# Performance work log

Hardware: AMD Instinct MI355X
Metric: run time of the kernel (lower is better)

Reference implementation:

```python
import jax, jax.numpy as jnp
import numpy as np

EPS = 1e-12  # torch F.normalize default eps


def conv1x1(x, w, b):
    # x: [N,C,H,W], w: [K,C], b: [K]
    return jnp.einsum('nchw,kc->nkhw', x, w) + b[None, :, None, None]


def forward_sa(f1, f2, cw1, cb1, cw2, cb2):
    n, _, h, w = f1.shape
    c1 = conv1x1(f1, cw1, cb1)  # [N,1,H,W]
    c2 = conv1x1(f2, cw2, cb2)
    c1 = jax.nn.softmax(c1.reshape(n, h * w), axis=1).reshape(n, 1, h, w)
    c2 = jax.nn.softmax(c2.reshape(n, h * w), axis=1).reshape(n, 1, h, w)
    return c1 * f1, c2 * f2


def l2norm_ch(x):
    # torch F.normalize(x) -> p=2 over dim=1 with eps clamp
    n = jnp.sqrt(jnp.sum(x * x, axis=1, keepdims=True))
    return x / jnp.maximum(n, EPS)


def forward_ca(f1, f2, pw1, pb1, pw2, pb2):
    N, C, H, W = f1.shape
    f1_cl = conv1x1(f1, pw1, pb1).reshape(N, -1, H * W)  # [N,Cl,HW]
    f2_cl = conv1x1(f2, pw2, pb2).reshape(N, -1, H * W)
    # A[n,p,q] = sum_c f2_cl[n,c,p] * f1_cl[n,c,q]  -> [N,HW,HW]
    A_c = jnp.tanh(jnp.einsum('ncp,ncq->npq', f2_cl, f1_cl))
    f1_v = f1.reshape(N, C, H * W)
    f2_v = f2.reshape(N, C, H * W)
    # f1_hat = f1_v @ A_c^T ; f2_hat = f2_v @ A_c
    f1_hat = jnp.einsum('ncp,nqp->ncq', f1_v, A_c).reshape(N, C, H, W)
    f2_hat = jnp.einsum('ncp,npq->ncq', f2_v, A_c).reshape(N, C, H, W)
    return l2norm_ch(f1_hat), l2norm_ch(f2_hat)


def setup_inputs() -> dict:
    key = jax.random.key(0)
    ks = jax.random.split(key, 10)
    N, C, H, W = 2, 256, 64, 64
    Cl = C // 16
    sc = 1.0 / np.sqrt(C)
    return {
        'f1': jax.random.normal(ks[0], (N, C, H, W), jnp.float32),
        'f2': jax.random.normal(ks[1], (N, C, H, W), jnp.float32),
        'pw1': jax.random.normal(ks[2], (Cl, C), jnp.float32) * sc,
        'pb1': jax.random.normal(ks[3], (Cl,), jnp.float32) * sc,
        'pw2': jax.random.normal(ks[4], (Cl, C), jnp.float32) * sc,
        'pb2': jax.random.normal(ks[5], (Cl,), jnp.float32) * sc,
        'cw1': jax.random.normal(ks[6], (1, C), jnp.float32) * sc,
        'cb1': jax.random.normal(ks[7], (1,), jnp.float32) * sc,
        'cw2': jax.random.normal(ks[8], (1, C), jnp.float32) * sc,
        'cb2': jax.random.normal(ks[9], (1,), jnp.float32) * sc,
    }


def reference(f1, f2, pw1, pb1, pw2, pb2, cw1, cb1, cw2, cb2):
    f1_1, f2_1 = forward_sa(f1, f2, cw1, cb1, cw2, cb2)
    f1_hat, f2_hat = forward_ca(f1_1, f2_1, pw1, pb1, pw2, pb2)
    fp1_hat = jax.nn.relu(f1_hat + f1)
    fp2_hat = jax.nn.relu(f2_hat + f2)
    f1_2, f2_2 = forward_sa(fp1_hat, fp2_hat, cw1, cb1, cw2, cb2)
    # Original calls forward_ca(f1_2, f2_2) again but discards the result
    # and returns (f1_2, f2_2); the dead call is omitted (identical output).
    return (f1_2, f2_2)
```

## Files before the change

### kernel.cpp

```cpp
#include <hip/hip_runtime.h>
#include <hip/hip_bf16.h>
#include <math.h>

#define N_B 2
#define C_CH 256
#define HW_SZ 4096
#define CL_CH 16

typedef __bf16 bf16x8 __attribute__((ext_vector_type(8)));
typedef float f32x4 __attribute__((ext_vector_type(4)));
typedef float f32x16 __attribute__((ext_vector_type(16)));

__device__ __forceinline__ unsigned short f2bf(float x){
  __hip_bfloat16 b = __float2bfloat16(x);
  return *reinterpret_cast<unsigned short*>(&b);
}
__device__ __forceinline__ float bf2f(unsigned short u){
  unsigned int w = ((unsigned int)u) << 16;
  return *reinterpret_cast<float*>(&w);
}
__device__ __forceinline__ unsigned int cvtpk(float a, float b){
  unsigned int r;
  asm("v_cvt_pk_bf16_f32 %0, %1, %2" : "=v"(r) : "v"(a), "v"(b));
  return r;
}
__device__ __forceinline__ float tanh_fast(float x){
  float e = __expf(2.0f * x);
  return fmaf(-2.0f, __builtin_amdgcn_rcpf(1.0f + e), 1.0f);
}
__device__ __forceinline__ void gload16(const void* gsrc, void* lds_dst){
  __builtin_amdgcn_global_load_lds(
      (const __attribute__((address_space(1))) unsigned int*)gsrc,
      (__attribute__((address_space(3))) unsigned int*)lds_dst, 16, 0, 0);
}

__global__ void k_conv1(const float* __restrict__ f1, const float* __restrict__ f2,
                        const float* __restrict__ w1, const float* __restrict__ w2,
                        const float* __restrict__ b1, const float* __restrict__ b2,
                        float* __restrict__ cv){
  const int i = blockIdx.z, n = blockIdx.y, t = threadIdx.x;
  const int ql = t & 63, cg = t >> 6;
  const int q = blockIdx.x * 64 + ql;
  const float* f = (i ? f2 : f1) + n * C_CH * HW_SZ;
  const float* w = i ? w2 : w1;
  __shared__ float ws[C_CH];
  __shared__ float red[4][72];
  ws[t] = w[t];
  __syncthreads();
  float acc = 0.f;
  #pragma unroll 8
  for (int c = cg * 64; c < cg * 64 + 64; ++c)
    acc += f[c * HW_SZ + q] * ws[c];
  red[cg][ql] = acc;
  __syncthreads();
  if (t < 64){
    float s = red[0][t] + red[1][t] + red[2][t] + red[3][t] + (i ? b2[0] : b1[0]);
    cv[(i * 2 + n) * HW_SZ + blockIdx.x * 64 + t] = s;
  }
}

__global__ void k_scale_cl(const float* __restrict__ f1, const float* __restrict__ f2,
                           const float* __restrict__ cv,
                           const float* __restrict__ pw1, const float* __restrict__ pw2,
                           const float* __restrict__ pb1, const float* __restrict__ pb2,
                           unsigned short* __restrict__ fs1, unsigned short* __restrict__ fs2,
                           unsigned short* __restrict__ clT1, unsigned short* __restrict__ clT2){
  const int i = blockIdx.z, n = blockIdx.y, t = threadIdx.x;
  const int ql = t & 63, cg = t >> 6;
  const int q = blockIdx.x * 64 + ql;
  const float* f = (i ? f2 : f1) + n * C_CH * HW_SZ;
  unsigned short* fs = (i ? fs2 : fs1) + n * C_CH * HW_SZ;
  unsigned short* clT = (i ? clT2 : clT1) + n * 32 * HW_SZ;
  const float* pw = i ? pw2 : pw1;
  const float* pb = i ? pb2 : pb1;
  const float* cvrow = cv + (i * 2 + n) * HW_SZ;
  __shared__ float wls[CL_CH * C_CH];
  __shared__ float red[4][CL_CH][66];
  __shared__ float smr[256];
  #pragma unroll
  for (int j = 0; j < 16; j++) wls[j * 256 + t] = pw[j * 256 + t];
  float sv[16];
  float m = -1e30f;
  #pragma unroll
  for (int j = 0; j < 16; j++){ sv[j] = cvrow[j * 256 + t]; m = fmaxf(m, sv[j]); }
  smr[t] = m; __syncthreads();
  for (int s = 128; s > 0; s >>= 1){ if (t < s) smr[t] = fmaxf(smr[t], smr[t + s]); __syncthreads(); }
  m = smr[0]; __syncthreads();
  float sum = 0.f;
  #pragma unroll
  for (int j = 0; j < 16; j++) sum += __expf(sv[j] - m);
  smr[t] = sum; __syncthreads();
  for (int s = 128; s > 0; s >>= 1){ if (t < s) smr[t] += smr[t + s]; __syncthreads(); }
  const float p = __expf(cvrow[q] - m) * (1.0f / smr[0]);

  float acc[16];
  #pragma unroll
  for (int k = 0; k < 16; k++) acc[k] = 0.f;
  for (int c = cg * 64; c < cg * 64 + 64; ++c){
    float vv = f[c * HW_SZ + q] * p;
    fs[c * HW_SZ + q] = f2bf(vv);
    #pragma unroll
    for (int k = 0; k < 16; k++) acc[k] += wls[k * 256 + c] * vv;
  }
  #pragma unroll
  for (int k = 0; k < 16; k++) red[cg][k][ql] = acc[k];
  __syncthreads();
  #pragma unroll
  for (int j = 0; j < 4; j++){
    int e = j * 256 + t; int k = e >> 6, qq = e & 63;
    float s = red[0][k][qq] + red[1][k][qq] + red[2][k][qq] + red[3][k][qq] + pb[k];
    clT[(blockIdx.x * 64 + qq) * 32 + k] = f2bf(s);
  }
  if (t < 128){
    uint4 zv = {0u, 0u, 0u, 0u};
    int qq = t >> 1, half = t & 1;
    *reinterpret_cast<uint4*>(&clT[(blockIdx.x * 64 + qq) * 32 + 16 + half * 8]) = zv;
  }
}

__global__ __launch_bounds__(512, 2) void k_hat(
    const unsigned short* __restrict__ fs1, const unsigned short* __restrict__ fs2,
    const unsigned short* __restrict__ clT1, const unsigned short* __restrict__ clT2,
    float* __restrict__ hat1, float* __restrict__ hat2,
    float* __restrict__ pt1, float* __restrict__ pt2){
  const int t = threadIdx.x;
  const int bid = blockIdx.x;
  const int xcd = bid & 7, slot = bid >> 3;
  const int z = xcd >> 1;
  const int n = z & 1, i = z >> 1;
  const int x = slot * 2 + (xcd & 1);
  const int qt = x >> 1, ph = x & 1;
  const int q0 = qt * 128;
  const int pbase = ph * 2048;

  const unsigned short* fs = (i ? fs2 : fs1) + n * C_CH * HW_SZ;
  const unsigned short* uT = (i ? clT1 : clT2) + n * 32 * HW_SZ;
  const unsigned short* vT = (i ? clT2 : clT1) + n * 32 * HW_SZ;
  float* out = (ph ? (i ? pt2 : pt1) : (i ? hat2 : hat1)) + n * C_CH * HW_SZ;

  __shared__ __align__(16) unsigned short fsA[3][C_CH * 64];
  __shared__ __align__(16) unsigned short aT[3][128 * 64];

  const int wv = t >> 6, l = t & 63;
  const int g4 = l >> 4, lr16 = l & 15;
  const int g2 = l >> 5, lr32 = l & 31;

  const int pfw = wv & 3;
  const int qh  = wv >> 2;
  const int cblk = wv & 3, qblk = wv >> 2;

  bf16x8 ub[4];
  #pragma unroll
  for (int j = 0; j < 4; ++j)
    ub[j] = *reinterpret_cast<const bf16x8*>(&uT[(q0 + qh * 64 + j * 16 + lr16) * 32 + g4 * 8]);

  f32x16 acc00, acc01, acc10, acc11;
  #pragma unroll
  for (int r = 0; r < 16; ++r){ acc00[r] = 0.f; acc01[r] = 0.f; acc10[r] = 0.f; acc11[r] = 0.f; }
  const f32x4 zz = {0.f, 0.f, 0.f, 0.f};

  int fs_src[4];
  #pragma unroll
  for (int it = 0; it < 4; ++it){
    int d = it * 512 + t; int c = d >> 3, sl = d & 7;
    int u = sl ^ (c & 7) ^ (((c >> 3) & 1) << 2) ^ (((c >> 4) & 1) << 1);
    fs_src[it] = c * (HW_SZ * 2) + u * 16;
  }
  const int vgo = (pfw * 16 + lr16) * 64 + g4 * 16;
  unsigned atw0;
  {
    int qd = qh * 64 + lr16;
    int sw = (pfw * 2 + (g4 >> 1)) ^ (qd & 7) ^ (((qd >> 3) & 1) << 2);
    atw0 = qd * 128 + sw * 16 + (g4 & 1) * 8;
  }
  unsigned afo[2], bqo[2];
  #pragma unroll
  for (int cf = 0; cf < 2; ++cf){
    int crow = cblk * 64 + cf * 32 + lr32;
    afo[cf] = crow * 128 +
      ((g2 ^ (crow & 7) ^ (((crow >> 3) & 1) << 2) ^ (((crow >> 4) & 1) << 1)) << 4);
  }
  #pragma unroll
  for (int qf = 0; qf < 2; ++qf){
    int qrow = qblk * 64 + qf * 32 + lr32;
    bqo[qf] = qrow * 128 +
      ((g2 ^ (qrow & 7) ^ (((qrow >> 3) & 1) << 2) ^ (((qrow >> 4) & 1) << 1)) << 4);
  }

  auto stage_fs = [&](char* dstbase, const char* src){
    #pragma unroll
    for (int it = 0; it < 4; ++it)
      gload16(src + fs_src[it], dstbase + (it * 512 + wv * 64) * 16);
  };
  auto dgen = [&](uint4 vr, char* atB){
    bf16x8 av = *reinterpret_cast<bf16x8*>(&vr);
    #pragma unroll
    for (int j = 0; j < 4; ++j){
      f32x4 d = __builtin_amdgcn_mfma_f32_16x16x32_bf16(av, ub[j], zz, 0, 0, 0);
      uint2 pk;
      pk.x = cvtpk(tanh_fast(d[0]), tanh_fast(d[1]));
      pk.y = cvtpk(tanh_fast(d[2]), tanh_fast(d[3]));
      unsigned off = (atw0 + (unsigned)(j * 2048)) ^ ((unsigned)(j & 1) << 5);
      *reinterpret_cast<uint2*>(atB + off) = pk;
    }
  };
  auto mmain = [&](const char* faB, const char* atB){
    __builtin_amdgcn_s_setprio(1);
    #pragma unroll
    for (int ks = 0; ks < 4; ++ks){
      unsigned kx = (unsigned)(ks << 5);
      bf16x8 a0 = *reinterpret_cast<const bf16x8*>(faB + (afo[0] ^ kx));
      bf16x8 a1 = *reinterpret_cast<const bf16x8*>(faB + (afo[1] ^ kx));
      bf16x8 b0 = *reinterpret_cast<const bf16x8*>(atB + (bqo[0] ^ kx));
      bf16x8 b1 = *reinterpret_cast<const bf16x8*>(atB + (bqo[1] ^ kx));
      acc00 = __builtin_amdgcn_mfma_f32_32x32x16_bf16(a0, b0, acc00, 0, 0, 0);
      acc01 = __builtin_amdgcn_mfma_f32_32x32x16_bf16(a0, b1, acc01, 0, 0, 0);
      acc10 = __builtin_amdgcn_mfma_f32_32x32x16_bf16(a1, b0, acc10, 0, 0, 0);
      acc11 = __builtin_amdgcn_mfma_f32_32x32x16_bf16(a1, b1, acc11, 0, 0, 0);
    }
    __builtin_amdgcn_s_setprio(0);
  };

  const char* fpp = (const char*)fs + pbase * 2;
  const char* vp  = (const char*)vT + pbase * 64 + vgo;

  char *fRd = (char*)&fsA[0][0], *fWr = (char*)&fsA[1][0], *fSp = (char*)&fsA[2][0];
  char *aRd = (char*)&aT[0][0],  *aWr = (char*)&aT[1][0],  *aSp = (char*)&aT[2][0];

  stage_fs(fRd, fpp); fpp += 128;
  uint4 vb;
  {
    uint4 va = *reinterpret_cast<const uint4*>(vp);
    vb = *reinterpret_cast<const uint4*>(vp + 4096);
    vp += 8192;
    dgen(va, aRd);
  }

  #pragma unroll 1
  for (int k = 0; k < 32; ++k){
    stage_fs(fWr, fpp); fpp += 128;
    uint4 vnew = *reinterpret_cast<const uint4*>(vp); vp += 4096;
    dgen(vb, aWr);
    vb = vnew;
    asm volatile("s_waitcnt lgkmcnt(0)" ::: "memory");
    __builtin_amdgcn_sched_barrier(0);
    __builtin_amdgcn_s_barrier();
    __builtin_amdgcn_sched_barrier(0);
    mmain(fRd, aRd);
    char* tf = fRd; fRd = fWr; fWr = fSp; fSp = tf;
    char* ta = aRd; aRd = aWr; aWr = aSp; aSp = ta;
  }

  const int qcol = q0 + qblk * 64 + lr32;
  #pragma unroll
  for (int r = 0; r < 16; ++r){
    int cr = (r & 3) + 8 * (r >> 2) + 4 * g2;
    out[(cblk * 64 + cr) * HW_SZ + qcol] = acc00[r];
    out[(cblk * 64 + cr) * HW_SZ + qcol + 32] = acc01[r];
    out[(cblk * 64 + 32 + cr) * HW_SZ + qcol] = acc10[r];
    out[(cblk * 64 + 32 + cr) * HW_SZ + qcol + 32] = acc11[r];
  }
}

__global__ void k_norm(const float* __restrict__ hat1, const float* __restrict__ hat2,
                       const float* __restrict__ pt1, const float* __restrict__ pt2,
                       const float* __restrict__ f1, const float* __restrict__ f2,
                       const float* __restrict__ cw1, const float* __restrict__ cw2,
                       const float* __restrict__ cb1, const float* __restrict__ cb2,
                       unsigned short* __restrict__ fpb1, unsigned short* __restrict__ fpb2,
                       float* __restrict__ cv2){
  const int i = blockIdx.z, n = blockIdx.y, t = threadIdx.x;
  const int ql = t & 63, cg = t >> 6;
  const int q = blockIdx.x * 64 + ql;
  const float* hat = (i ? hat2 : hat1) + n * C_CH * HW_SZ;
  const float* pt = (i ? pt2 : pt1) + n * C_CH * HW_SZ;
  const float* f = (i ? f2 : f1) + n * C_CH * HW_SZ;
  unsigned short* fpb = (i ? fpb2 : fpb1) + n * C_CH * HW_SZ;
  __shared__ float ws[C_CH];
  __shared__ float red[4][72];
  __shared__ float invs[64];
  __shared__ unsigned short hLs[C_CH][66];
  ws[t] = (i ? cw2 : cw1)[t];
  __syncthreads();
  float s = 0.f;
  #pragma unroll 8
  for (int c = cg * 64; c < cg * 64 + 64; ++c){
    float h = hat[c * HW_SZ + q] + pt[c * HW_SZ + q];
    hLs[c][ql] = f2bf(h);
    s += h * h;
  }
  red[cg][ql] = s; __syncthreads();
  if (t < 64){
    float ss = red[0][t] + red[1][t] + red[2][t] + red[3][t];
    invs[t] = 1.0f / fmaxf(sqrtf(ss), 1e-12f);
  }
  __syncthreads();
  const float inv = invs[ql];
  float ca = 0.f;
  #pragma unroll 8
  for (int c = cg * 64; c < cg * 64 + 64; ++c){
    float vv = fmaxf(bf2f(hLs[c][ql]) * inv + f[c * HW_SZ + q], 0.0f);
    fpb[c * HW_SZ + q] = f2bf(vv);
    ca += ws[c] * vv;
  }
  red[cg][ql] = ca; __syncthreads();
  if (t < 64){
    float ss = red[0][t] + red[1][t] + red[2][t] + red[3][t] + (i ? cb2[0] : cb1[0]);
    cv2[(i * 2 + n) * HW_SZ + blockIdx.x * 64 + t] = ss;
  }
}

__global__ void k_final(const unsigned short* __restrict__ fp1,
                        const unsigned short* __restrict__ fp2,
                        const float* __restrict__ cv2, float* __restrict__ outp){
  const int i = blockIdx.z, t = threadIdx.x;
  const int idx4 = (blockIdx.x * 256 + t) * 4;
  const int n = idx4 >> 20;
  const int q = idx4 & (HW_SZ - 1);
  const float* cvrow = cv2 + (i * 2 + n) * HW_SZ;
  __shared__ float red[256];
  float sv[16];
  float m = -1e30f;
  #pragma unroll
  for (int j = 0; j < 16; j++){ sv[j] = cvrow[j * 256 + t]; m = fmaxf(m, sv[j]); }
  red[t] = m; __syncthreads();
  for (int s = 128; s > 0; s >>= 1){ if (t < s) red[t] = fmaxf(red[t], red[t + s]); __syncthreads(); }
  m = red[0]; __syncthreads();
  float sum = 0.f;
  #pragma unroll
  for (int j = 0; j < 16; j++) sum += __expf(sv[j] - m);
  red[t] = sum; __syncthreads();
  for (int s = 128; s > 0; s >>= 1){ if (t < s) red[t] += red[t + s]; __syncthreads(); }
  const float invS = 1.0f / red[0];

  const unsigned short* fp = i ? fp2 : fp1;
  ushort4 vv = *reinterpret_cast<const ushort4*>(&fp[idx4]);
  float4 o;
  o.x = bf2f(vv.x) * (__expf(cvrow[q + 0] - m) * invS);
  o.y = bf2f(vv.y) * (__expf(cvrow[q + 1] - m) * invS);
  o.z = bf2f(vv.z) * (__expf(cvrow[q + 2] - m) * invS);
  o.w = bf2f(vv.w) * (__expf(cvrow[q + 3] - m) * invS);
  *reinterpret_cast<float4*>(&outp[i * (C_CH * HW_SZ * N_B) + idx4]) = o;
}

extern "C" void kernel_launch(void* const* d_in, const int* in_sizes, int n_in,
                              void* d_out, int out_size, void* d_ws, size_t ws_size,
                              hipStream_t stream){
  const float* f1  = (const float*)d_in[0];
  const float* f2  = (const float*)d_in[1];
  const float* pw1 = (const float*)d_in[2];
  const float* pb1 = (const float*)d_in[3];
  const float* pw2 = (const float*)d_in[4];
  const float* pb2 = (const float*)d_in[5];
  const float* cw1 = (const float*)d_in[6];
  const float* cb1 = (const float*)d_in[7];
  const float* cw2 = (const float*)d_in[8];
  const float* cb2 = (const float*)d_in[9];
  float* ws = (float*)d_ws;
  float* HAT1 = ws;
  float* HAT2 = ws + 2097152;
  float* PT1  = ws + 4194304;
  float* PT2  = ws + 6291456;
  unsigned short* FS1 = (unsigned short*)(ws + 8388608);
  unsigned short* FS2 = (unsigned short*)(ws + 9437184);
  unsigned short* CLT1 = (unsigned short*)(ws + 10485760);
  unsigned short* CLT2 = (unsigned short*)(ws + 10616832);
  float* CV1  = ws + 10747904;
  float* CV2  = ws + 10764288;
  float* outp = (float*)d_out;
  unsigned short* FPB1 = FS1;
  unsigned short* FPB2 = FS2;

  k_conv1   <<<dim3(64, 2, 2), 256, 0, stream>>>(f1, f2, cw1, cw2, cb1, cb2, CV1);
  k_scale_cl<<<dim3(64, 2, 2), 256, 0, stream>>>(f1, f2, CV1, pw1, pw2, pb1, pb2,
                                                 FS1, FS2, CLT1, CLT2);
  k_hat     <<<256, 512, 0, stream>>>(FS1, FS2, CLT1, CLT2, HAT1, HAT2, PT1, PT2);
  k_norm    <<<dim3(64, 2, 2), 256, 0, stream>>>(HAT1, HAT2, PT1, PT2, f1, f2,
                                                 cw1, cw2, cb1, cb2, FPB1, FPB2, CV2);
  k_final   <<<dim3(2048, 1, 2), 256, 0, stream>>>(FPB1, FPB2, CV2, outp);
}
```

Measured before the change: 96.72 us.

## Store hat partials as bf16 and reorder MFMA before dgen in k_hat loop

The k_hat partial outputs (hat and pt) are now written and read as bf16 instead of fp32, which halves the intermediate HBM traffic between k_hat and k_norm. The main loop is reordered so that mmain on the current buffers runs before generating the next attention tile, with an extra barrier before the loop. The s_setprio hints are removed. Storing partials in bf16 adds rounding error before they are summed, and the reordering changes how MFMA work overlaps with tanh and LDS writes.

```diff
diff --git a/kernel.cpp b/kernel.cpp
--- a/kernel.cpp
+++ b/kernel.cpp
@@ -121,8 +121,8 @@
 __global__ __launch_bounds__(512, 2) void k_hat(
     const unsigned short* __restrict__ fs1, const unsigned short* __restrict__ fs2,
     const unsigned short* __restrict__ clT1, const unsigned short* __restrict__ clT2,
-    float* __restrict__ hat1, float* __restrict__ hat2,
-    float* __restrict__ pt1, float* __restrict__ pt2){
+    unsigned short* __restrict__ hat1, unsigned short* __restrict__ hat2,
+    unsigned short* __restrict__ pt1, unsigned short* __restrict__ pt2){
   const int t = threadIdx.x;
   const int bid = blockIdx.x;
   const int xcd = bid & 7, slot = bid >> 3;
@@ -136,7 +136,7 @@
   const unsigned short* fs = (i ? fs2 : fs1) + n * C_CH * HW_SZ;
   const unsigned short* uT = (i ? clT1 : clT2) + n * 32 * HW_SZ;
   const unsigned short* vT = (i ? clT2 : clT1) + n * 32 * HW_SZ;
-  float* out = (ph ? (i ? pt2 : pt1) : (i ? hat2 : hat1)) + n * C_CH * HW_SZ;
+  unsigned short* out = (ph ? (i ? pt2 : pt1) : (i ? hat2 : hat1)) + n * C_CH * HW_SZ;
 
   __shared__ __align__(16) unsigned short fsA[3][C_CH * 64];
   __shared__ __align__(16) unsigned short aT[3][128 * 64];
@@ -205,7 +205,6 @@
     }
   };
   auto mmain = [&](const char* faB, const char* atB){
-    __builtin_amdgcn_s_setprio(1);
     #pragma unroll
     for (int ks = 0; ks < 4; ++ks){
       unsigned kx = (unsigned)(ks << 5);
@@ -218,7 +217,6 @@
       acc10 = __builtin_amdgcn_mfma_f32_32x32x16_bf16(a1, b0, acc10, 0, 0, 0);
       acc11 = __builtin_amdgcn_mfma_f32_32x32x16_bf16(a1, b1, acc11, 0, 0, 0);
     }
-    __builtin_amdgcn_s_setprio(0);
   };
 
   const char* fpp = (const char*)fs + pbase * 2;
@@ -235,18 +233,22 @@
     vp += 8192;
     dgen(va, aRd);
   }
+  asm volatile("s_waitcnt lgkmcnt(0)" ::: "memory");
+  __builtin_amdgcn_sched_barrier(0);
+  __builtin_amdgcn_s_barrier();
+  __builtin_amdgcn_sched_barrier(0);
 
   #pragma unroll 1
   for (int k = 0; k < 32; ++k){
     stage_fs(fWr, fpp); fpp += 128;
     uint4 vnew = *reinterpret_cast<const uint4*>(vp); vp += 4096;
+    mmain(fRd, aRd);
     dgen(vb, aWr);
     vb = vnew;
     asm volatile("s_waitcnt lgkmcnt(0)" ::: "memory");
     __builtin_amdgcn_sched_barrier(0);
     __builtin_amdgcn_s_barrier();
     __builtin_amdgcn_sched_barrier(0);
-    mmain(fRd, aRd);
     char* tf = fRd; fRd = fWr; fWr = fSp; fSp = tf;
     char* ta = aRd; aRd = aWr; aWr = aSp; aSp = ta;
   }
@@ -255,15 +257,17 @@
   #pragma unroll
   for (int r = 0; r < 16; ++r){
     int cr = (r & 3) + 8 * (r >> 2) + 4 * g2;
-    out[(cblk * 64 + cr) * HW_SZ + qcol] = acc00[r];
-    out[(cblk * 64 + cr) * HW_SZ + qcol + 32] = acc01[r];
-    out[(cblk * 64 + 32 + cr) * HW_SZ + qcol] = acc10[r];
-    out[(cblk * 64 + 32 + cr) * HW_SZ + qcol + 32] = acc11[r];
-  }
-}
-
-__global__ void k_norm(const float* __restrict__ hat1, const float* __restrict__ hat2,
-                       const float* __restrict__ pt1, const float* __restrict__ pt2,
+    out[(cblk * 64 + cr) * HW_SZ + qcol] = f2bf(acc00[r]);
+    out[(cblk * 64 + cr) * HW_SZ + qcol + 32] = f2bf(acc01[r]);
+    out[(cblk * 64 + 32 + cr) * HW_SZ + qcol] = f2bf(acc10[r]);
+    out[(cblk * 64 + 32 + cr) * HW_SZ + qcol + 32] = f2bf(acc11[r]);
+  }
+}
+
+__global__ void k_norm(const unsigned short* __restrict__ hat1,
+                       const unsigned short* __restrict__ hat2,
+                       const unsigned short* __restrict__ pt1,
+                       const unsigned short* __restrict__ pt2,
                        const float* __restrict__ f1, const float* __restrict__ f2,
                        const float* __restrict__ cw1, const float* __restrict__ cw2,
                        const float* __restrict__ cb1, const float* __restrict__ cb2,
@@ -272,8 +276,8 @@
   const int i = blockIdx.z, n = blockIdx.y, t = threadIdx.x;
   const int ql = t & 63, cg = t >> 6;
   const int q = blockIdx.x * 64 + ql;
-  const float* hat = (i ? hat2 : hat1) + n * C_CH * HW_SZ;
-  const float* pt = (i ? pt2 : pt1) + n * C_CH * HW_SZ;
+  const unsigned short* hat = (i ? hat2 : hat1) + n * C_CH * HW_SZ;
+  const unsigned short* pt = (i ? pt2 : pt1) + n * C_CH * HW_SZ;
   const float* f = (i ? f2 : f1) + n * C_CH * HW_SZ;
   unsigned short* fpb = (i ? fpb2 : fpb1) + n * C_CH * HW_SZ;
   __shared__ float ws[C_CH];
@@ -285,7 +289,7 @@
   float s = 0.f;
   #pragma unroll 8
   for (int c = cg * 64; c < cg * 64 + 64; ++c){
-    float h = hat[c * HW_SZ + q] + pt[c * HW_SZ + q];
+    float h = bf2f(hat[c * HW_SZ + q]) + bf2f(pt[c * HW_SZ + q]);
     hLs[c][ql] = f2bf(h);
     s += h * h;
   }
@@ -357,16 +361,16 @@
   const float* cw2 = (const float*)d_in[8];
   const float* cb2 = (const float*)d_in[9];
   float* ws = (float*)d_ws;
-  float* HAT1 = ws;
-  float* HAT2 = ws + 2097152;
-  float* PT1  = ws + 4194304;
-  float* PT2  = ws + 6291456;
-  unsigned short* FS1 = (unsigned short*)(ws + 8388608);
-  unsigned short* FS2 = (unsigned short*)(ws + 9437184);
-  unsigned short* CLT1 = (unsigned short*)(ws + 10485760);
-  unsigned short* CLT2 = (unsigned short*)(ws + 10616832);
-  float* CV1  = ws + 10747904;
-  float* CV2  = ws + 10764288;
+  unsigned short* HAT1 = (unsigned short*)(ws);
+  unsigned short* HAT2 = (unsigned short*)(ws + 1048576);
+  unsigned short* PT1  = (unsigned short*)(ws + 2097152);
+  unsigned short* PT2  = (unsigned short*)(ws + 3145728);
+  unsigned short* FS1  = (unsigned short*)(ws + 4194304);
+  unsigned short* FS2  = (unsigned short*)(ws + 5242880);
+  unsigned short* CLT1 = (unsigned short*)(ws + 6291456);
+  unsigned short* CLT2 = (unsigned short*)(ws + 6553600);
+  float* CV1  = ws + 6815744;
+  float* CV2  = ws + 6832128;
   float* outp = (float*)d_out;
   unsigned short* FPB1 = FS1;
   unsigned short* FPB2 = FS2;
```

New measurement: 99.05 us. +2.4%, slower.
